# Kernel optimization log

Hardware: AMD Instinct MI355X
Metric: run time of the kernel (lower is better)

Reference implementation:

```python
import jax, jax.numpy as jnp
import numpy as np

IN_FEATURES = 4096
OUT_FEATURES = 4096
DISTANCE_FACTOR = 64


def make_band_mask(out_features, in_features, d):
    rows = jnp.arange(out_features)[:, None]
    cols = jnp.arange(in_features)[None, :]
    return (jnp.abs(rows - cols) <= d).astype(jnp.float32)


def setup_inputs() -> dict:
    key = jax.random.key(0)
    k_x, k_w, k_b = jax.random.split(key, 3)
    x = jax.random.normal(k_x, (8192, IN_FEATURES), dtype=jnp.float32)
    # kaiming_uniform_(a=sqrt(5)) on [out, in]: bound = sqrt(6/((1+5)*fan_in)) = 1/sqrt(fan_in)
    bound_w = 1.0 / np.sqrt(IN_FEATURES)
    weight = jax.random.uniform(k_w, (OUT_FEATURES, IN_FEATURES), dtype=jnp.float32,
                                minval=-bound_w, maxval=bound_w)
    bound_b = 1.0 / np.sqrt(IN_FEATURES)
    bias = jax.random.uniform(k_b, (OUT_FEATURES,), dtype=jnp.float32,
                              minval=-bound_b, maxval=bound_b)
    mask = make_band_mask(OUT_FEATURES, IN_FEATURES, DISTANCE_FACTOR)
    return {"x": x, "weight": weight, "bias": bias, "mask": mask}


def reference(x, weight, bias, mask):
    # masked banded weight, then dense linear: y = x @ (mask*W)^T + b
    masked_weight = mask * weight  # [out, in]
    return jnp.einsum('bi,oi->bo', x, masked_weight) + bias
```

## Files before the change

### kernel.cpp

```cpp
#include <hip/hip_runtime.h>
#include <hip/hip_bf16.h>
#include <stdint.h>


constexpr int MROWS = 8192;
constexpr int NFEAT = 4096;
constexpr int KFEAT = 4096;
constexpr int DBAND = 64;

constexpr int BM = 128;
constexpr int BN = 128;
constexpr int BK = 64;
constexpr int KT = BN + 2 * DBAND;
constexpr int NCH = KT / BK;
constexpr int LDSW = BK + 8;

using bf16x8 = __attribute__((ext_vector_type(8))) short;
using f32x4  = __attribute__((ext_vector_type(4))) float;

__device__ __forceinline__ uint32_t pk2(float a, float b) {
    float2 t; t.x = a; t.y = b;
    __hip_bfloat162 h = __float22bfloat162_rn(t);
    union { __hip_bfloat162 h; uint32_t u; } cv;
    cv.h = h;
    return cv.u;
}

__global__ __launch_bounds__(256)
void band_linear_kernel(const float* __restrict__ x,
                        const float* __restrict__ w,
                        const float* __restrict__ bias,
                        float* __restrict__ y)
{
    __shared__ __align__(16) short sA[BM * LDSW];
    __shared__ __align__(16) short sB[BN * LDSW];

    const int tid  = threadIdx.x;
    const int lane = tid & 63;
    const int wave = tid >> 6;
    const int wm = wave & 1;
    const int wn = wave >> 1;

    const int cb = blockIdx.x;
    const int rb = blockIdx.y;
    const int row0 = rb * BM;
    const int col0 = cb * BN;
    const int i0 = col0 - DBAND;

    const int srow = tid >> 1;
    const int koff = (tid & 1) * (BK / 2);

    const int gn  = col0 + srow;
    const int wlo = gn - DBAND;
    const int whi = gn + DBAND;

    f32x4 acc[4][4];
    #pragma unroll
    for (int i = 0; i < 4; ++i)
        #pragma unroll
        for (int j = 0; j < 4; ++j)
            acc[i][j] = (f32x4){0.f, 0.f, 0.f, 0.f};

    const float* xsrc = x + (size_t)(row0 + srow) * KFEAT;
    const float* wsrc = w + (size_t)gn * KFEAT;

    for (int ch = 0; ch < NCH; ++ch) {
        const int kbase = i0 + ch * BK;
        if (kbase < 0 || kbase >= KFEAT) continue;

        #pragma unroll
        for (int g = 0; g < 4; ++g) {
            const int kk = koff + g * 8;
            const float4 v0 = *(const float4*)(xsrc + kbase + kk);
            const float4 v1 = *(const float4*)(xsrc + kbase + kk + 4);
            uint4 p;
            p.x = pk2(v0.x, v0.y);
            p.y = pk2(v0.z, v0.w);
            p.z = pk2(v1.x, v1.y);
            p.w = pk2(v1.z, v1.w);
            *(uint4*)&sA[srow * LDSW + kk] = p;
        }

        #pragma unroll
        for (int g = 0; g < 4; ++g) {
            const int kk = koff + g * 8;
            const int gk = kbase + kk;
            float4 v0 = *(const float4*)(wsrc + gk);
            float4 v1 = *(const float4*)(wsrc + gk + 4);
            v0.x = (gk + 0 >= wlo && gk + 0 <= whi) ? v0.x : 0.f;
            v0.y = (gk + 1 >= wlo && gk + 1 <= whi) ? v0.y : 0.f;
            v0.z = (gk + 2 >= wlo && gk + 2 <= whi) ? v0.z : 0.f;
            v0.w = (gk + 3 >= wlo && gk + 3 <= whi) ? v0.w : 0.f;
            v1.x = (gk + 4 >= wlo && gk + 4 <= whi) ? v1.x : 0.f;
            v1.y = (gk + 5 >= wlo && gk + 5 <= whi) ? v1.y : 0.f;
            v1.z = (gk + 6 >= wlo && gk + 6 <= whi) ? v1.z : 0.f;
            v1.w = (gk + 7 >= wlo && gk + 7 <= whi) ? v1.w : 0.f;
            uint4 p;
            p.x = pk2(v0.x, v0.y);
            p.y = pk2(v0.z, v0.w);
            p.z = pk2(v1.x, v1.y);
            p.w = pk2(v1.z, v1.w);
            *(uint4*)&sB[srow * LDSW + kk] = p;
        }

        __syncthreads();

        #pragma unroll
        for (int s = 0; s < 2; ++s) {
            bf16x8 af[4], bfr[4];
            #pragma unroll
            for (int mf = 0; mf < 4; ++mf) {
                const int r = wm * 64 + mf * 16 + (lane & 15);
                af[mf] = *(const bf16x8*)&sA[r * LDSW + s * 32 + (lane >> 4) * 8];
            }
            #pragma unroll
            for (int nf = 0; nf < 4; ++nf) {
                const int r = wn * 64 + nf * 16 + (lane & 15);
                bfr[nf] = *(const bf16x8*)&sB[r * LDSW + s * 32 + (lane >> 4) * 8];
            }
            #pragma unroll
            for (int mf = 0; mf < 4; ++mf)
                #pragma unroll
                for (int nf = 0; nf < 4; ++nf)
                    acc[mf][nf] = __builtin_amdgcn_mfma_f32_16x16x32_bf16(
                        af[mf], bfr[nf], acc[mf][nf], 0, 0, 0);
        }

        __syncthreads();
    }

    const int lquad = lane >> 4;
    const int lcol  = lane & 15;
    #pragma unroll
    for (int nf = 0; nf < 4; ++nf) {
        const int gc = col0 + wn * 64 + nf * 16 + lcol;
        const float bv = bias[gc];
        #pragma unroll
        for (int mf = 0; mf < 4; ++mf) {
            const int gr = row0 + wm * 64 + mf * 16 + lquad * 4;
            float* dst = y + (size_t)gr * NFEAT + gc;
            #pragma unroll
            for (int r2 = 0; r2 < 4; ++r2)
                dst[(size_t)r2 * NFEAT] = acc[mf][nf][r2] + bv;
        }
    }
}

extern "C" void kernel_launch(void* const* d_in, const int* in_sizes, int n_in,
                              void* d_out, int out_size, void* d_ws, size_t ws_size,
                              hipStream_t stream) {
    const float* x    = (const float*)d_in[0];
    const float* w    = (const float*)d_in[1];
    const float* bias = (const float*)d_in[2];
    float* y = (float*)d_out;

    dim3 grid(NFEAT / BN, MROWS / BM);
    band_linear_kernel<<<grid, 256, 0, stream>>>(x, w, bias, y);
}
```

Measured before the change: 332.6 us.

## Double the block to 512 threads and register-prefetch the next K chunk

Each block now runs 8 waves instead of 4. Every wave computes a 64x32 sub-tile, and each thread stages 16 elements per chunk instead of 32. Global loads for the next K chunk are issued into registers right after the barrier, so they overlap the MFMA work on the current chunk. The out-of-range edge chunks are dropped from the loop bounds instead of being skipped each iteration. The costs are more register pressure from the prefetch buffers and more threads per block, which may limit occupancy.

```diff
diff --git a/kernel.cpp b/kernel.cpp
--- a/kernel.cpp
+++ b/kernel.cpp
@@ -11,8 +11,7 @@
 constexpr int BM = 128;
 constexpr int BN = 128;
 constexpr int BK = 64;
-constexpr int KT = BN + 2 * DBAND;
-constexpr int NCH = KT / BK;
+constexpr int NCH = (BN + 2 * DBAND) / BK;
 constexpr int LDSW = BK + 8;
 
 using bf16x8 = __attribute__((ext_vector_type(8))) short;
@@ -26,7 +25,7 @@
     return cv.u;
 }
 
-__global__ __launch_bounds__(256)
+__global__ __launch_bounds__(512)
 void band_linear_kernel(const float* __restrict__ x,
                         const float* __restrict__ w,
                         const float* __restrict__ bias,
@@ -38,8 +37,8 @@
     const int tid  = threadIdx.x;
     const int lane = tid & 63;
     const int wave = tid >> 6;
-    const int wm = wave & 1;
-    const int wn = wave >> 1;
+    const int wm = wave >> 2;
+    const int wn = wave & 3;
 
     const int cb = blockIdx.x;
     const int rb = blockIdx.y;
@@ -47,93 +46,109 @@
     const int col0 = cb * BN;
     const int i0 = col0 - DBAND;
 
-    const int srow = tid >> 1;
-    const int koff = (tid & 1) * (BK / 2);
+    const int srow = tid >> 2;
+    const int koff = (tid & 3) * 16;
 
     const int gn  = col0 + srow;
     const int wlo = gn - DBAND;
     const int whi = gn + DBAND;
 
-    f32x4 acc[4][4];
+    const float* xsrc = x + (size_t)(row0 + srow) * KFEAT + koff;
+    const float* wsrc = w + (size_t)gn * KFEAT + koff;
+
+    f32x4 acc[4][2];
     #pragma unroll
     for (int i = 0; i < 4; ++i)
         #pragma unroll
-        for (int j = 0; j < 4; ++j)
+        for (int j = 0; j < 2; ++j)
             acc[i][j] = (f32x4){0.f, 0.f, 0.f, 0.f};
 
-    const float* xsrc = x + (size_t)(row0 + srow) * KFEAT;
-    const float* wsrc = w + (size_t)gn * KFEAT;
+    float4 px[4], pw[4];
 
-    for (int ch = 0; ch < NCH; ++ch) {
-        const int kbase = i0 + ch * BK;
-        if (kbase < 0 || kbase >= KFEAT) continue;
+    int ch = (cb == 0) ? 1 : 0;
+    const int che = (cb == (NFEAT / BN - 1)) ? (NCH - 1) : NCH;
 
+    {
+        const int kb = i0 + ch * BK;
         #pragma unroll
         for (int g = 0; g < 4; ++g) {
-            const int kk = koff + g * 8;
-            const float4 v0 = *(const float4*)(xsrc + kbase + kk);
-            const float4 v1 = *(const float4*)(xsrc + kbase + kk + 4);
-            uint4 p;
-            p.x = pk2(v0.x, v0.y);
-            p.y = pk2(v0.z, v0.w);
-            p.z = pk2(v1.x, v1.y);
-            p.w = pk2(v1.z, v1.w);
-            *(uint4*)&sA[srow * LDSW + kk] = p;
+            px[g] = *(const float4*)(xsrc + kb + g * 4);
+            pw[g] = *(const float4*)(wsrc + kb + g * 4);
         }
+    }
 
-        #pragma unroll
-        for (int g = 0; g < 4; ++g) {
-            const int kk = koff + g * 8;
-            const int gk = kbase + kk;
-            float4 v0 = *(const float4*)(wsrc + gk);
-            float4 v1 = *(const float4*)(wsrc + gk + 4);
-            v0.x = (gk + 0 >= wlo && gk + 0 <= whi) ? v0.x : 0.f;
-            v0.y = (gk + 1 >= wlo && gk + 1 <= whi) ? v0.y : 0.f;
-            v0.z = (gk + 2 >= wlo && gk + 2 <= whi) ? v0.z : 0.f;
-            v0.w = (gk + 3 >= wlo && gk + 3 <= whi) ? v0.w : 0.f;
-            v1.x = (gk + 4 >= wlo && gk + 4 <= whi) ? v1.x : 0.f;
-            v1.y = (gk + 5 >= wlo && gk + 5 <= whi) ? v1.y : 0.f;
-            v1.z = (gk + 6 >= wlo && gk + 6 <= whi) ? v1.z : 0.f;
-            v1.w = (gk + 7 >= wlo && gk + 7 <= whi) ? v1.w : 0.f;
-            uint4 p;
-            p.x = pk2(v0.x, v0.y);
-            p.y = pk2(v0.z, v0.w);
-            p.z = pk2(v1.x, v1.y);
-            p.w = pk2(v1.z, v1.w);
-            *(uint4*)&sB[srow * LDSW + kk] = p;
+    while (true) {
+        {
+            const int kg = i0 + ch * BK + koff;
+            uint4 pa0, pa1, pb0, pb1;
+            pa0.x = pk2(px[0].x, px[0].y);  pa0.y = pk2(px[0].z, px[0].w);
+            pa0.z = pk2(px[1].x, px[1].y);  pa0.w = pk2(px[1].z, px[1].w);
+            pa1.x = pk2(px[2].x, px[2].y);  pa1.y = pk2(px[2].z, px[2].w);
+            pa1.z = pk2(px[3].x, px[3].y);  pa1.w = pk2(px[3].z, px[3].w);
+            float4 mv[4];
+            #pragma unroll
+            for (int g = 0; g < 4; ++g) {
+                const int gk = kg + g * 4;
+                float4 v = pw[g];
+                v.x = (gk + 0 >= wlo && gk + 0 <= whi) ? v.x : 0.f;
+                v.y = (gk + 1 >= wlo && gk + 1 <= whi) ? v.y : 0.f;
+                v.z = (gk + 2 >= wlo && gk + 2 <= whi) ? v.z : 0.f;
+                v.w = (gk + 3 >= wlo && gk + 3 <= whi) ? v.w : 0.f;
+                mv[g] = v;
+            }
+            pb0.x = pk2(mv[0].x, mv[0].y);  pb0.y = pk2(mv[0].z, mv[0].w);
+            pb0.z = pk2(mv[1].x, mv[1].y);  pb0.w = pk2(mv[1].z, mv[1].w);
+            pb1.x = pk2(mv[2].x, mv[2].y);  pb1.y = pk2(mv[2].z, mv[2].w);
+            pb1.z = pk2(mv[3].x, mv[3].y);  pb1.w = pk2(mv[3].z, mv[3].w);
+            *(uint4*)&sA[srow * LDSW + koff]     = pa0;
+            *(uint4*)&sA[srow * LDSW + koff + 8] = pa1;
+            *(uint4*)&sB[srow * LDSW + koff]     = pb0;
+            *(uint4*)&sB[srow * LDSW + koff + 8] = pb1;
         }
 
         __syncthreads();
 
+        const bool more = (ch + 1) < che;
+        if (more) {
+            const int kb = i0 + (ch + 1) * BK;
+            #pragma unroll
+            for (int g = 0; g < 4; ++g) {
+                px[g] = *(const float4*)(xsrc + kb + g * 4);
+                pw[g] = *(const float4*)(wsrc + kb + g * 4);
+            }
+        }
+
         #pragma unroll
         for (int s = 0; s < 2; ++s) {
-            bf16x8 af[4], bfr[4];
+            bf16x8 af[4], bfr[2];
             #pragma unroll
             for (int mf = 0; mf < 4; ++mf) {
                 const int r = wm * 64 + mf * 16 + (lane & 15);
                 af[mf] = *(const bf16x8*)&sA[r * LDSW + s * 32 + (lane >> 4) * 8];
             }
             #pragma unroll
-            for (int nf = 0; nf < 4; ++nf) {
-                const int r = wn * 64 + nf * 16 + (lane & 15);
+            for (int nf = 0; nf < 2; ++nf) {
+                const int r = wn * 32 + nf * 16 + (lane & 15);
                 bfr[nf] = *(const bf16x8*)&sB[r * LDSW + s * 32 + (lane >> 4) * 8];
             }
             #pragma unroll
             for (int mf = 0; mf < 4; ++mf)
                 #pragma unroll
-                for (int nf = 0; nf < 4; ++nf)
+                for (int nf = 0; nf < 2; ++nf)
                     acc[mf][nf] = __builtin_amdgcn_mfma_f32_16x16x32_bf16(
                         af[mf], bfr[nf], acc[mf][nf], 0, 0, 0);
         }
 
+        if (!more) break;
         __syncthreads();
+        ++ch;
     }
 
     const int lquad = lane >> 4;
     const int lcol  = lane & 15;
     #pragma unroll
-    for (int nf = 0; nf < 4; ++nf) {
-        const int gc = col0 + wn * 64 + nf * 16 + lcol;
+    for (int nf = 0; nf < 2; ++nf) {
+        const int gc = col0 + wn * 32 + nf * 16 + lcol;
         const float bv = bias[gc];
         #pragma unroll
         for (int mf = 0; mf < 4; ++mf) {
@@ -155,5 +170,5 @@
     float* y = (float*)d_out;
 
     dim3 grid(NFEAT / BN, MROWS / BM);
-    band_linear_kernel<<<grid, 256, 0, stream>>>(x, w, bias, y);
+    band_linear_kernel<<<grid, 512, 0, stream>>>(x, w, bias, y);
 }
```

After: 300.1 us. 9.8% less time.
